# Optimization experiments

Hardware: AMD Instinct MI355X
Metric: run time of the kernel (lower is better)

## Reference

```python
import jax, jax.numpy as jnp
import numpy as np

BN_EPS = 1e-5

def _conv(x, w, b=None, pad=0):
    # x: NCHW, w: OIHW
    y = jax.lax.conv_general_dilated(x, w, (1, 1), [(pad, pad), (pad, pad)],
                                     dimension_numbers=('NCHW', 'OIHW', 'NCHW'))
    if b is not None:
        y = y + b[None, :, None, None]
    return y

def setup_inputs() -> dict:
    key = jax.random.key(0)
    ks = jax.random.split(key, 16)
    B, C, H, W = 8, 10, 128, 128
    IN_DIM = 256
    inp = {
        'f_node': jax.random.normal(ks[0], (B, C, H, W), jnp.float32),
        'h_node0': jax.random.normal(ks[1], (B, C, H, W), jnp.float32),
        'h_node1': jax.random.normal(ks[2], (B, C, H, W), jnp.float32),
        'p_nodes': jax.random.normal(ks[3], (6, B, C, H, W), jnp.float32),
        'xf': jax.random.normal(ks[4], (B, IN_DIM, H, W), jnp.float32),
        # Comp_att: 1x1 conv (2*C -> 1) + bias, then sigmoid
        'att_w': jax.random.normal(ks[5], (1, 2 * C, 1, 1), jnp.float32) * 0.1,
        'att_b': jnp.zeros((1,), jnp.float32),
        # Composition: 3x3 conv (2*C -> C), no bias; BatchNorm (eval-mode stats)
        'rel_w': jax.random.normal(ks[6], (C, 2 * C, 3, 3), jnp.float32) * 0.1,
        'bn_gamma': jnp.ones((C,), jnp.float32),
        'bn_beta': jnp.zeros((C,), jnp.float32),
        'bn_mean': jnp.zeros((C,), jnp.float32),
        'bn_var': jnp.ones((C,), jnp.float32),
        # ConvGRU (1x1 kernels): gates conv (2*C -> 2*C), candidate conv (2*C -> C)
        'gates_w': jax.random.normal(ks[7], (2 * C, 2 * C, 1, 1), jnp.float32) * 0.1,
        'gates_b': jnp.zeros((2 * C,), jnp.float32),
        'can_w': jax.random.normal(ks[8], (C, 2 * C, 1, 1), jnp.float32) * 0.1,
        'can_b': jnp.zeros((C,), jnp.float32),
    }
    return inp

def reference(f_node, h_node0, h_node1, p_nodes, xf,
              att_w, att_b, rel_w, bn_gamma, bn_beta, bn_mean, bn_var,
              gates_w, gates_b, can_w, can_b):
    C = f_node.shape[1]
    # --- Comp_att: sigmoid(1x1 conv over concat of children) -> [B,1,H,W]
    comp_att = jax.nn.sigmoid(_conv(jnp.concatenate([h_node0, h_node1], axis=1), att_w, att_b))
    # --- Composition: sum over children of ReLU(BN(conv3x3(cat[parent, child*att])))
    inv_std = bn_gamma / jnp.sqrt(bn_var + BN_EPS)
    def relation(child):
        y = _conv(jnp.concatenate([f_node, child * comp_att], axis=1), rel_w, pad=1)
        y = (y - bn_mean[None, :, None, None]) * inv_std[None, :, None, None] + bn_beta[None, :, None, None]
        return jax.nn.relu(y)
    comp_h = relation(h_node0) + relation(h_node1)
    # --- ConvGRU update (single step, 1x1 convs): input=comp_h, hidden=f_node
    combined = jnp.concatenate([comp_h, f_node], axis=1)
    gates = _conv(combined, gates_w, gates_b)
    reset = jax.nn.sigmoid(gates[:, :C])
    update = jax.nn.sigmoid(gates[:, C:])
    cand = jnp.tanh(_conv(jnp.concatenate([comp_h, reset * f_node], axis=1), can_w, can_b))
    f_node_new = (1.0 - update) * f_node + update * cand
    return (f_node_new, comp_att)
```

## Files before the change

### kernel.cpp

```cpp
#include <hip/hip_runtime.h>

#define B_   8
#define C_   10
#define H_   128
#define W_   128
#define HWSZ (H_ * W_)
#define CHW  (C_ * HWSZ)

#define TS   16
#define HL   18
#define HST  19
#define HSZ  (HL * HL)
#define NTHREADS 128

__device__ __forceinline__ float sigm(float x)  { return 1.0f / (1.0f + __expf(-x)); }
__device__ __forceinline__ float tanh_(float x) { return 1.0f - 2.0f / (__expf(2.0f * x) + 1.0f); }

__global__ __launch_bounds__(NTHREADS) void fused_graph_kernel(
    const float* __restrict__ f_g,
    const float* __restrict__ h0_g,
    const float* __restrict__ h1_g,
    const float* __restrict__ attw_g,
    const float* __restrict__ attb_g,
    const float* __restrict__ relw_g,
    const float* __restrict__ gamma_g,
    const float* __restrict__ beta_g,
    const float* __restrict__ mean_g,
    const float* __restrict__ var_g,
    const float* __restrict__ gw_g,
    const float* __restrict__ gb_g,
    const float* __restrict__ cw_g,
    const float* __restrict__ cb_g,
    float* __restrict__ out_f,
    float* __restrict__ out_att)
{
    __shared__ float sF [C_][HL * HST];
    __shared__ float sA0[C_][HL * HST];
    __shared__ float sA1[C_][HL * HST];
    __shared__ float sAtt[HL * HST];
    __shared__ float sWf[9][10][12];
    __shared__ float sWa[9][10][12];
    __shared__ float sGW[20][20];
    __shared__ float sCW[20][12];
    __shared__ float sGB[20], sCB[10], sSc[10], sBi[10];

    const int tid = threadIdx.x;
    const int bx = blockIdx.x, by = blockIdx.y, b = blockIdx.z;

    for (int i = tid; i < 900; i += NTHREADS) {
        const int tap = i / 100, r = i - tap * 100, ci = r / 10, c = r - ci * 10;
        sWf[tap][ci][c] = relw_g[(c * 20 + ci) * 9 + tap];
        sWa[tap][ci][c] = relw_g[(c * 20 + 10 + ci) * 9 + tap];
    }
    for (int i = tid; i < 400; i += NTHREADS) {
        const int in_c = i / 20, o = i - in_c * 20;
        sGW[in_c][o] = gw_g[o * 20 + in_c];
    }
    for (int i = tid; i < 200; i += NTHREADS) {
        const int in_c = i / 10, c = i - in_c * 10;
        sCW[in_c][c] = cw_g[c * 20 + in_c];
    }
    if (tid < 20) sGB[tid] = gb_g[tid];
    if (tid < 10) {
        sCB[tid] = cb_g[tid];
        const float sc = gamma_g[tid] * rsqrtf(var_g[tid] + 1e-5f);
        sSc[tid] = sc;
        sBi[tid] = beta_g[tid] - mean_g[tid] * sc;
    }

    float aw[20];
    #pragma unroll
    for (int i = 0; i < 20; i++) aw[i] = attw_g[i];
    const float ab = attb_g[0];

    const int gy0 = by * TS - 1, gx0 = bx * TS - 1;
    for (int p = tid; p < HSZ; p += NTHREADS) {
        const int hy = p / HL, hx = p - hy * HL;
        const int gy = gy0 + hy, gx = gx0 + hx;
        const int q = hy * HST + hx;
        if (gy >= 0 && gy < H_ && gx >= 0 && gx < W_) {
            const int base = b * CHW + gy * W_ + gx;
            float h0v[10], h1v[10];
            float acc = ab;
            #pragma unroll
            for (int ci = 0; ci < 10; ci++) {
                h0v[ci] = h0_g[base + ci * HWSZ];
                h1v[ci] = h1_g[base + ci * HWSZ];
                acc += aw[ci] * h0v[ci] + aw[10 + ci] * h1v[ci];
            }
            const float att = sigm(acc);
            sAtt[q] = att;
            #pragma unroll
            for (int ci = 0; ci < 10; ci++) {
                sF [ci][q] = f_g[base + ci * HWSZ];
                sA0[ci][q] = h0v[ci] * att;
                sA1[ci][q] = h1v[ci] * att;
            }
        } else {
            sAtt[q] = 0.0f;
            #pragma unroll
            for (int ci = 0; ci < 10; ci++) { sF[ci][q] = 0.0f; sA0[ci][q] = 0.0f; sA1[ci][q] = 0.0f; }
        }
    }
    __syncthreads();

    const int ly = tid >> 3, lxp = tid & 7;
    const int hc = (ly + 1) * HST + (2 * lxp + 1);

    float accf[2][10], acc0[2][10], acc1[2][10];
    #pragma unroll
    for (int c = 0; c < 10; c++) {
        accf[0][c] = 0.f; accf[1][c] = 0.f;
        acc0[0][c] = 0.f; acc0[1][c] = 0.f;
        acc1[0][c] = 0.f; acc1[1][c] = 0.f;
    }

    #pragma unroll 1
    for (int tap = 0; tap < 9; tap++) {
        const int dy = tap / 3 - 1, dx = tap - (tap / 3) * 3 - 1;
        const int hi = hc + dy * HST + dx;
        #pragma unroll
        for (int ci = 0; ci < 10; ci++) {
            const float f0 = sF [ci][hi], f1 = sF [ci][hi + 1];
            const float p0 = sA0[ci][hi], p1 = sA0[ci][hi + 1];
            const float q0 = sA1[ci][hi], q1 = sA1[ci][hi + 1];
            #pragma unroll
            for (int c = 0; c < 10; c++) {
                const float wfv = sWf[tap][ci][c];
                const float wav = sWa[tap][ci][c];
                accf[0][c] += wfv * f0; accf[1][c] += wfv * f1;
                acc0[0][c] += wav * p0; acc0[1][c] += wav * p1;
                acc1[0][c] += wav * q0; acc1[1][c] += wav * q1;
            }
        }
    }

    const int gy = by * TS + ly, gx = bx * TS + 2 * lxp;
    float fnew[2][10];
    #pragma unroll
    for (int px = 0; px < 2; px++) {
        float ch[10], fc[10];
        #pragma unroll
        for (int c = 0; c < 10; c++) {
            const float y0 = (accf[px][c] + acc0[px][c]) * sSc[c] + sBi[c];
            const float y1 = (accf[px][c] + acc1[px][c]) * sSc[c] + sBi[c];
            ch[c] = fmaxf(y0, 0.f) + fmaxf(y1, 0.f);
            fc[c] = sF[c][hc + px];
        }
        float g[20];
        #pragma unroll
        for (int o = 0; o < 20; o++) g[o] = sGB[o];
        #pragma unroll
        for (int i = 0; i < 10; i++) {
            #pragma unroll
            for (int o = 0; o < 20; o++)
                g[o] += ch[i] * sGW[i][o] + fc[i] * sGW[10 + i][o];
        }
        float cd[10];
        #pragma unroll
        for (int c = 0; c < 10; c++) cd[c] = sCB[c];
        #pragma unroll
        for (int i = 0; i < 10; i++) {
            const float rf = sigm(g[i]) * fc[i];
            #pragma unroll
            for (int c = 0; c < 10; c++)
                cd[c] += ch[i] * sCW[i][c] + rf * sCW[10 + i][c];
        }
        #pragma unroll
        for (int c = 0; c < 10; c++) {
            const float u = sigm(g[10 + c]);
            fnew[px][c] = (1.f - u) * fc[c] + u * tanh_(cd[c]);
        }
    }

    #pragma unroll
    for (int c = 0; c < 10; c++) {
        float2 v = make_float2(fnew[0][c], fnew[1][c]);
        *reinterpret_cast<float2*>(&out_f[((b * C_ + c) * H_ + gy) * W_ + gx]) = v;
    }
    {
        float2 v = make_float2(sAtt[hc], sAtt[hc + 1]);
        *reinterpret_cast<float2*>(&out_att[(b * H_ + gy) * W_ + gx]) = v;
    }
}

extern "C" void kernel_launch(void* const* d_in, const int* in_sizes, int n_in,
                              void* d_out, int out_size, void* d_ws, size_t ws_size,
                              hipStream_t stream) {
    (void)in_sizes; (void)n_in; (void)d_ws; (void)ws_size; (void)out_size;
    const float* f   = (const float*)d_in[0];
    const float* h0  = (const float*)d_in[1];
    const float* h1  = (const float*)d_in[2];
    const float* aw  = (const float*)d_in[5];
    const float* ab  = (const float*)d_in[6];
    const float* rw  = (const float*)d_in[7];
    const float* gam = (const float*)d_in[8];
    const float* bet = (const float*)d_in[9];
    const float* mea = (const float*)d_in[10];
    const float* var = (const float*)d_in[11];
    const float* gw  = (const float*)d_in[12];
    const float* gb  = (const float*)d_in[13];
    const float* cw  = (const float*)d_in[14];
    const float* cb  = (const float*)d_in[15];

    float* out_f   = (float*)d_out;
    float* out_att = out_f + (B_ * C_ * H_ * W_);

    dim3 grid(W_ / TS, H_ / TS, B_);
    fused_graph_kernel<<<grid, dim3(NTHREADS), 0, stream>>>(
        f, h0, h1, aw, ab, rw, gam, bet, mea, var, gw, gb, cw, cb, out_f, out_att);
}
```

Before: 242.8 us.

## Precompute folded weights in prep kernel, pack inputs as float4 tiles, one pixel per thread

A small prep kernel folds the BatchNorm scale into the 3x3 weights and writes all weights to a workspace buffer. The main kernel then reads them straight from global memory with uniform addresses instead of staging them in shared memory per block. The three input tiles and the attention map are interleaved into one float4 shared array, so each tap needs a single 128-bit LDS read. Threads go from 128 to 256 with one pixel each, which lowers register pressure and raises occupancy, at the cost of an extra launch and losing two-pixel weight reuse.

```diff
diff --git a/kernel.cpp b/kernel.cpp
--- a/kernel.cpp
+++ b/kernel.cpp
@@ -11,67 +11,75 @@
 #define HL   18
 #define HST  19
 #define HSZ  (HL * HL)
-#define NTHREADS 128
+#define NTHREADS 256
+
+#define WOFF_W3 0
+#define WOFF_BI 1800
+#define WOFF_AW 1810
+#define WOFF_AB 1830
+#define WOFF_GW 1832
+#define WOFF_GB 2232
+#define WOFF_CW 2252
+#define WOFF_CB 2452
 
 __device__ __forceinline__ float sigm(float x)  { return 1.0f / (1.0f + __expf(-x)); }
 __device__ __forceinline__ float tanh_(float x) { return 1.0f - 2.0f / (__expf(2.0f * x) + 1.0f); }
+
+__global__ __launch_bounds__(256) void prep_kernel(
+    const float* __restrict__ attw, const float* __restrict__ attb,
+    const float* __restrict__ relw,
+    const float* __restrict__ gamma, const float* __restrict__ beta,
+    const float* __restrict__ mean,  const float* __restrict__ var,
+    const float* __restrict__ gw, const float* __restrict__ gb,
+    const float* __restrict__ cw, const float* __restrict__ cb,
+    float* __restrict__ ws)
+{
+    const int tid = threadIdx.x;
+    for (int i = tid; i < 1800; i += 256) {
+        const int g20 = i / 20, j = i - g20 * 20;
+        const int tap = g20 / 10, ci = g20 - tap * 10;
+        const int c   = (j < 10) ? j : j - 10;
+        const int cin = (j < 10) ? ci : 10 + ci;
+        const float sc = gamma[c] * rsqrtf(var[c] + 1e-5f);
+        ws[WOFF_W3 + i] = relw[(c * 20 + cin) * 9 + tap] * sc;
+    }
+    if (tid < 10) {
+        const float sc = gamma[tid] * rsqrtf(var[tid] + 1e-5f);
+        ws[WOFF_BI + tid] = beta[tid] - mean[tid] * sc;
+        ws[WOFF_CB + tid] = cb[tid];
+    }
+    if (tid < 20) {
+        ws[WOFF_AW + tid] = attw[tid];
+        ws[WOFF_GB + tid] = gb[tid];
+    }
+    if (tid == 0) ws[WOFF_AB] = attb[0];
+    for (int i = tid; i < 400; i += 256) {
+        const int ic = i / 20, o = i - ic * 20;
+        ws[WOFF_GW + i] = gw[o * 20 + ic];
+    }
+    for (int i = tid; i < 200; i += 256) {
+        const int ic = i / 10, c = i - ic * 10;
+        ws[WOFF_CW + i] = cw[c * 20 + ic];
+    }
+}
 
 __global__ __launch_bounds__(NTHREADS) void fused_graph_kernel(
     const float* __restrict__ f_g,
     const float* __restrict__ h0_g,
     const float* __restrict__ h1_g,
-    const float* __restrict__ attw_g,
-    const float* __restrict__ attb_g,
-    const float* __restrict__ relw_g,
-    const float* __restrict__ gamma_g,
-    const float* __restrict__ beta_g,
-    const float* __restrict__ mean_g,
-    const float* __restrict__ var_g,
-    const float* __restrict__ gw_g,
-    const float* __restrict__ gb_g,
-    const float* __restrict__ cw_g,
-    const float* __restrict__ cb_g,
+    const float* __restrict__ ws,
     float* __restrict__ out_f,
     float* __restrict__ out_att)
 {
-    __shared__ float sF [C_][HL * HST];
-    __shared__ float sA0[C_][HL * HST];
-    __shared__ float sA1[C_][HL * HST];
-    __shared__ float sAtt[HL * HST];
-    __shared__ float sWf[9][10][12];
-    __shared__ float sWa[9][10][12];
-    __shared__ float sGW[20][20];
-    __shared__ float sCW[20][12];
-    __shared__ float sGB[20], sCB[10], sSc[10], sBi[10];
+    __shared__ float4 sIn[C_][HL * HST];
 
     const int tid = threadIdx.x;
     const int bx = blockIdx.x, by = blockIdx.y, b = blockIdx.z;
 
-    for (int i = tid; i < 900; i += NTHREADS) {
-        const int tap = i / 100, r = i - tap * 100, ci = r / 10, c = r - ci * 10;
-        sWf[tap][ci][c] = relw_g[(c * 20 + ci) * 9 + tap];
-        sWa[tap][ci][c] = relw_g[(c * 20 + 10 + ci) * 9 + tap];
-    }
-    for (int i = tid; i < 400; i += NTHREADS) {
-        const int in_c = i / 20, o = i - in_c * 20;
-        sGW[in_c][o] = gw_g[o * 20 + in_c];
-    }
-    for (int i = tid; i < 200; i += NTHREADS) {
-        const int in_c = i / 10, c = i - in_c * 10;
-        sCW[in_c][c] = cw_g[c * 20 + in_c];
-    }
-    if (tid < 20) sGB[tid] = gb_g[tid];
-    if (tid < 10) {
-        sCB[tid] = cb_g[tid];
-        const float sc = gamma_g[tid] * rsqrtf(var_g[tid] + 1e-5f);
-        sSc[tid] = sc;
-        sBi[tid] = beta_g[tid] - mean_g[tid] * sc;
-    }
-
     float aw[20];
     #pragma unroll
-    for (int i = 0; i < 20; i++) aw[i] = attw_g[i];
-    const float ab = attb_g[0];
+    for (int i = 0; i < 20; i++) aw[i] = ws[WOFF_AW + i];
+    const float ab = ws[WOFF_AB];
 
     const int gy0 = by * TS - 1, gx0 = bx * TS - 1;
     for (int p = tid; p < HSZ; p += NTHREADS) {
@@ -80,114 +88,93 @@
         const int q = hy * HST + hx;
         if (gy >= 0 && gy < H_ && gx >= 0 && gx < W_) {
             const int base = b * CHW + gy * W_ + gx;
-            float h0v[10], h1v[10];
+            float fv[10], h0v[10], h1v[10];
             float acc = ab;
             #pragma unroll
             for (int ci = 0; ci < 10; ci++) {
+                fv[ci]  = f_g [base + ci * HWSZ];
                 h0v[ci] = h0_g[base + ci * HWSZ];
                 h1v[ci] = h1_g[base + ci * HWSZ];
                 acc += aw[ci] * h0v[ci] + aw[10 + ci] * h1v[ci];
             }
             const float att = sigm(acc);
-            sAtt[q] = att;
-            #pragma unroll
-            for (int ci = 0; ci < 10; ci++) {
-                sF [ci][q] = f_g[base + ci * HWSZ];
-                sA0[ci][q] = h0v[ci] * att;
-                sA1[ci][q] = h1v[ci] * att;
-            }
+            #pragma unroll
+            for (int ci = 0; ci < 10; ci++)
+                sIn[ci][q] = make_float4(fv[ci], h0v[ci] * att, h1v[ci] * att, att);
         } else {
-            sAtt[q] = 0.0f;
-            #pragma unroll
-            for (int ci = 0; ci < 10; ci++) { sF[ci][q] = 0.0f; sA0[ci][q] = 0.0f; sA1[ci][q] = 0.0f; }
+            #pragma unroll
+            for (int ci = 0; ci < 10; ci++)
+                sIn[ci][q] = make_float4(0.f, 0.f, 0.f, 0.f);
         }
     }
     __syncthreads();
 
-    const int ly = tid >> 3, lxp = tid & 7;
-    const int hc = (ly + 1) * HST + (2 * lxp + 1);
-
-    float accf[2][10], acc0[2][10], acc1[2][10];
-    #pragma unroll
-    for (int c = 0; c < 10; c++) {
-        accf[0][c] = 0.f; accf[1][c] = 0.f;
-        acc0[0][c] = 0.f; acc0[1][c] = 0.f;
-        acc1[0][c] = 0.f; acc1[1][c] = 0.f;
-    }
+    const int ly = tid >> 4, lx = tid & 15;
+    const int hc = (ly + 1) * HST + (lx + 1);
+
+    float accf[10], acc0[10], acc1[10];
+    #pragma unroll
+    for (int c = 0; c < 10; c++) { accf[c] = 0.f; acc0[c] = 0.f; acc1[c] = 0.f; }
 
     #pragma unroll 1
     for (int tap = 0; tap < 9; tap++) {
-        const int dy = tap / 3 - 1, dx = tap - (tap / 3) * 3 - 1;
-        const int hi = hc + dy * HST + dx;
+        const int hi = hc + (tap / 3 - 1) * HST + (tap - (tap / 3) * 3 - 1);
         #pragma unroll
         for (int ci = 0; ci < 10; ci++) {
-            const float f0 = sF [ci][hi], f1 = sF [ci][hi + 1];
-            const float p0 = sA0[ci][hi], p1 = sA0[ci][hi + 1];
-            const float q0 = sA1[ci][hi], q1 = sA1[ci][hi + 1];
+            const float4 v = sIn[ci][hi];
+            const float* __restrict__ wp = ws + WOFF_W3 + (tap * 10 + ci) * 20;
             #pragma unroll
             for (int c = 0; c < 10; c++) {
-                const float wfv = sWf[tap][ci][c];
-                const float wav = sWa[tap][ci][c];
-                accf[0][c] += wfv * f0; accf[1][c] += wfv * f1;
-                acc0[0][c] += wav * p0; acc0[1][c] += wav * p1;
-                acc1[0][c] += wav * q0; acc1[1][c] += wav * q1;
+                accf[c] += wp[c]      * v.x;
+                acc0[c] += wp[10 + c] * v.y;
+                acc1[c] += wp[10 + c] * v.z;
             }
         }
     }
 
-    const int gy = by * TS + ly, gx = bx * TS + 2 * lxp;
-    float fnew[2][10];
-    #pragma unroll
-    for (int px = 0; px < 2; px++) {
-        float ch[10], fc[10];
+    float ch[10], fc[10], attv = 0.f;
+    #pragma unroll
+    for (int c = 0; c < 10; c++) {
+        const float4 cv = sIn[c][hc];
+        fc[c] = cv.x;
+        if (c == 0) attv = cv.w;
+        const float bi = ws[WOFF_BI + c];
+        ch[c] = fmaxf(accf[c] + acc0[c] + bi, 0.f) + fmaxf(accf[c] + acc1[c] + bi, 0.f);
+    }
+
+    float g[20];
+    #pragma unroll
+    for (int o = 0; o < 20; o++) g[o] = ws[WOFF_GB + o];
+    #pragma unroll
+    for (int i = 0; i < 10; i++) {
         #pragma unroll
-        for (int c = 0; c < 10; c++) {
-            const float y0 = (accf[px][c] + acc0[px][c]) * sSc[c] + sBi[c];
-            const float y1 = (accf[px][c] + acc1[px][c]) * sSc[c] + sBi[c];
-            ch[c] = fmaxf(y0, 0.f) + fmaxf(y1, 0.f);
-            fc[c] = sF[c][hc + px];
-        }
-        float g[20];
+        for (int o = 0; o < 20; o++)
+            g[o] += ch[i] * ws[WOFF_GW + i * 20 + o] + fc[i] * ws[WOFF_GW + (10 + i) * 20 + o];
+    }
+    float cd[10];
+    #pragma unroll
+    for (int c = 0; c < 10; c++) cd[c] = ws[WOFF_CB + c];
+    #pragma unroll
+    for (int i = 0; i < 10; i++) {
+        const float rf = sigm(g[i]) * fc[i];
         #pragma unroll
-        for (int o = 0; o < 20; o++) g[o] = sGB[o];
-        #pragma unroll
-        for (int i = 0; i < 10; i++) {
-            #pragma unroll
-            for (int o = 0; o < 20; o++)
-                g[o] += ch[i] * sGW[i][o] + fc[i] * sGW[10 + i][o];
-        }
-        float cd[10];
-        #pragma unroll
-        for (int c = 0; c < 10; c++) cd[c] = sCB[c];
-        #pragma unroll
-        for (int i = 0; i < 10; i++) {
-            const float rf = sigm(g[i]) * fc[i];
-            #pragma unroll
-            for (int c = 0; c < 10; c++)
-                cd[c] += ch[i] * sCW[i][c] + rf * sCW[10 + i][c];
-        }
-        #pragma unroll
-        for (int c = 0; c < 10; c++) {
-            const float u = sigm(g[10 + c]);
-            fnew[px][c] = (1.f - u) * fc[c] + u * tanh_(cd[c]);
-        }
-    }
-
+        for (int c = 0; c < 10; c++)
+            cd[c] += ch[i] * ws[WOFF_CW + i * 10 + c] + rf * ws[WOFF_CW + (10 + i) * 10 + c];
+    }
+
+    const int gy = by * TS + ly, gx = bx * TS + lx;
     #pragma unroll
     for (int c = 0; c < 10; c++) {
-        float2 v = make_float2(fnew[0][c], fnew[1][c]);
-        *reinterpret_cast<float2*>(&out_f[((b * C_ + c) * H_ + gy) * W_ + gx]) = v;
-    }
-    {
-        float2 v = make_float2(sAtt[hc], sAtt[hc + 1]);
-        *reinterpret_cast<float2*>(&out_att[(b * H_ + gy) * W_ + gx]) = v;
-    }
+        const float u = sigm(g[10 + c]);
+        out_f[((b * C_ + c) * H_ + gy) * W_ + gx] = (1.f - u) * fc[c] + u * tanh_(cd[c]);
+    }
+    out_att[(b * H_ + gy) * W_ + gx] = attv;
 }
 
 extern "C" void kernel_launch(void* const* d_in, const int* in_sizes, int n_in,
                               void* d_out, int out_size, void* d_ws, size_t ws_size,
                               hipStream_t stream) {
-    (void)in_sizes; (void)n_in; (void)d_ws; (void)ws_size; (void)out_size;
+    (void)in_sizes; (void)n_in; (void)ws_size; (void)out_size;
     const float* f   = (const float*)d_in[0];
     const float* h0  = (const float*)d_in[1];
     const float* h1  = (const float*)d_in[2];
@@ -203,10 +190,12 @@
     const float* cw  = (const float*)d_in[14];
     const float* cb  = (const float*)d_in[15];
 
+    float* wsf     = (float*)d_ws;
     float* out_f   = (float*)d_out;
     float* out_att = out_f + (B_ * C_ * H_ * W_);
 
+    prep_kernel<<<1, 256, 0, stream>>>(aw, ab, rw, gam, bet, mea, var, gw, gb, cw, cb, wsf);
+
     dim3 grid(W_ / TS, H_ / TS, B_);
-    fused_graph_kernel<<<grid, dim3(NTHREADS), 0, stream>>>(
-        f, h0, h1, aw, ab, rw, gam, bet, mea, var, gw, gb, cw, cb, out_f, out_att);
+    fused_graph_kernel<<<grid, dim3(NTHREADS), 0, stream>>>(f, h0, h1, wsf, out_f, out_att);
 }
```

Result: no change. 241.8 us (-0.4%).
